# Kernel tuning notes

Hardware: AMD Instinct MI355X
Metric: run time of the kernel (lower is better)

Reference implementation:

```python
import jax, jax.numpy as jnp
import numpy as np

B, L, D = 4, 2048, 1024
H, DK, DV = 16, 64, 64
SCALE = float((4 * DK) ** 0.5)
EPS = 1e-6


def setup_inputs() -> dict:
    key = jax.random.key(0)
    ks = jax.random.split(key, 16)
    s_in = 1.0 / np.sqrt(D)
    inp = {}
    for i, name in enumerate(["q_a", "k_a", "v_a", "q_s", "k_s", "v_s"]):
        inp[name] = jax.random.normal(ks[i], (B, L, D), dtype=jnp.float32)
    # weights stored as [in, out] so projection is x @ W (equivalent math to nn.Linear)
    for j, name in enumerate(["Wqa", "Wka", "Wva", "Wqs", "Wks", "Wvs", "Wfc"]):
        inp[name] = jax.random.normal(ks[6 + j], (D, D), dtype=jnp.float32) * s_in
    inp["gamma"] = jnp.ones((D,), dtype=jnp.float32)
    inp["beta"] = jnp.zeros((D,), dtype=jnp.float32)
    return inp


def _proj(x, W, dh):
    # [B,L,D] @ [D, H*dh] -> [B,H,L,dh]
    return (x @ W).reshape(B, -1, H, dh).transpose(0, 2, 1, 3)


def reference(q_a, k_a, v_a, q_s, k_s, v_s, Wqa, Wka, Wva, Wqs, Wks, Wvs, Wfc, gamma, beta):
    residual = q_a + q_s
    qa = _proj(q_a, Wqa, DK)
    ka = _proj(k_a, Wka, DK)
    va = _proj(v_a, Wva, DV)
    qs = _proj(q_s, Wqs, DK)
    ks_ = _proj(k_s, Wks, DK)
    vs = _proj(v_s, Wvs, DV)
    # a2a + a2s + s2a + s2s == (qa+qs) @ (ka+ks)^T  (algebraic identity)
    q = qa + qs
    k = ka + ks_
    v = va + vs
    scores = jnp.einsum("bhqd,bhkd->bhqk", q, k) / SCALE
    attn = jax.nn.softmax(scores, axis=-1)  # dropout = identity (eval)
    out = jnp.einsum("bhqk,bhkd->bhqd", attn, v)  # [B,H,L,DV]
    out = out.transpose(0, 2, 1, 3).reshape(B, L, H * DV)
    out = out @ Wfc + residual
    mu = jnp.mean(out, axis=-1, keepdims=True)
    var = jnp.var(out, axis=-1, keepdims=True)
    out = (out - mu) * jax.lax.rsqrt(var + EPS) * gamma + beta
    return out
```

## Files before the change

### kernel.cpp

```cpp
#include <hip/hip_runtime.h>
#include <hip/hip_bf16.h>
#include <stdint.h>

typedef __attribute__((ext_vector_type(4))) float f32x4;
typedef __attribute__((ext_vector_type(16))) float f32x16;
typedef __attribute__((ext_vector_type(8))) short short8;
typedef __attribute__((ext_vector_type(2))) int int2v;

#define DEV static __device__ __forceinline__

DEV unsigned short f2bf(float f) {
  unsigned u = __float_as_uint(f);
  u += 0x7fffu + ((u >> 16) & 1u);
  return (unsigned short)(u >> 16);
}

DEV uint32_t cvtpk(float a, float b) {
  uint32_t r;
  asm("v_cvt_pk_bf16_f32 %0, %1, %2" : "=v"(r) : "v"(a), "v"(b));
  return r;
}

DEV int2v pl32(int a, int b) {
  return __builtin_amdgcn_permlane32_swap(a, b, false, false);
}

typedef const __attribute__((address_space(1))) void* gas_ptr;
typedef __attribute__((address_space(3))) void* las_ptr;

DEV void gload_lds16(const void* g, void* l) {
  __builtin_amdgcn_global_load_lds((gas_ptr)g, (las_ptr)l, 16, 0, 0);
}

struct CvtArgs {
  const float* in[6];
  unsigned short* out[6];
};

__global__ __launch_bounds__(256) void cvt_kernel(CvtArgs a, int n4) {
  const float* __restrict__ in = a.in[blockIdx.y];
  unsigned short* __restrict__ out = a.out[blockIdx.y];
  int idx = blockIdx.x * blockDim.x + threadIdx.x;
  int stride = gridDim.x * blockDim.x;
  for (int i = idx; i < n4; i += stride) {
    float4 v = reinterpret_cast<const float4*>(in)[i];
    ushort4 o;
    o.x = f2bf(v.x); o.y = f2bf(v.y); o.z = f2bf(v.z); o.w = f2bf(v.w);
    reinterpret_cast<ushort4*>(out)[i] = o;
  }
}

struct TcvtArgs {
  const float* src[7];
  unsigned short* dst[7];
  int stride[7];
  int koff[7];
};

__global__ __launch_bounds__(256) void tcvt_kernel(TcvtArgs a) {
  const int which = blockIdx.z;
  const float* __restrict__ src = a.src[which];
  unsigned short* __restrict__ dst = a.dst[which];
  const int dstStride = a.stride[which], kOff = a.koff[which];
  __shared__ float tile[32][33];
  int tx = threadIdx.x & 31;
  int ty = threadIdx.x >> 5;
  int n0 = blockIdx.x * 32;
  int k0 = blockIdx.y * 32;
#pragma unroll
  for (int i = 0; i < 4; i++)
    tile[ty + 8 * i][tx] = src[(size_t)(k0 + ty + 8 * i) * 1024 + n0 + tx];
  __syncthreads();
#pragma unroll
  for (int i = 0; i < 4; i++) {
    int n = n0 + ty + 8 * i;
    dst[(size_t)n * dstStride + kOff + k0 + tx] = f2bf(tile[tx][ty + 8 * i]);
  }
}

struct G3Args {
  const unsigned short* A1[3];
  const unsigned short* A2[3];
  const unsigned short* WT[3];
  unsigned short* out[3];
};

__global__ __launch_bounds__(256) void gemm3_kernel(G3Args g) {
  __shared__ unsigned short As[128 * 32];
  __shared__ unsigned short Bs[128 * 32];
  const int orig = blockIdx.x;
  const int swz = (orig & 7) * 192 + (orig >> 3);
  const int which = swz >> 9;
  const int bid = swz & 511;
  const unsigned short* __restrict__ A1 = g.A1[which];
  const unsigned short* __restrict__ A2 = g.A2[which];
  const unsigned short* __restrict__ WT = g.WT[which];
  unsigned short* __restrict__ outp = g.out[which];

  const int tid = threadIdx.x;
  const int lane = tid & 63;
  const int w = tid >> 6;
  const int mt = bid >> 3, nt = bid & 7;
  const int m0 = mt * 128, n0 = nt * 128;

  const int srow = (w << 4) + (lane >> 2);
  const int scol = (lane & 3) << 3;

  f32x4 zero4 = {0.f, 0.f, 0.f, 0.f};
  f32x4 acc[4][4];
#pragma unroll
  for (int mi = 0; mi < 4; mi++)
#pragma unroll
    for (int ni = 0; ni < 4; ni++) acc[mi][ni] = zero4;

  const int wr = w >> 1, wc = w & 1;
  const int arow = (wr << 6) + (lane & 15);
  const int brow = (wc << 6) + (lane & 15);
  const int kcol = (lane >> 4) << 3;

  for (int kt = 0; kt < 64; kt++) {
    const int kk = kt << 5;
    const unsigned short* Asrc;
    int ka;
    if (kk < 1024) { Asrc = A1; ka = kk; } else { Asrc = A2; ka = kk - 1024; }
#pragma unroll
    for (int p = 0; p < 2; p++) {
      const unsigned short* gp = Asrc + (size_t)(m0 + p * 64 + srow) * 1024 + ka + scol;
      gload_lds16(gp, &As[(p * 64 + srow) * 32 + scol]);
    }
#pragma unroll
    for (int p = 0; p < 2; p++) {
      const unsigned short* gp = WT + (size_t)(n0 + p * 64 + srow) * 2048 + kk + scol;
      gload_lds16(gp, &Bs[(p * 64 + srow) * 32 + scol]);
    }
    __syncthreads();

    short8 av[4], bv[4];
#pragma unroll
    for (int mi = 0; mi < 4; mi++)
      av[mi] = *reinterpret_cast<const short8*>(&As[(arow + mi * 16) * 32 + kcol]);
#pragma unroll
    for (int ni = 0; ni < 4; ni++)
      bv[ni] = *reinterpret_cast<const short8*>(&Bs[(brow + ni * 16) * 32 + kcol]);
#pragma unroll
    for (int mi = 0; mi < 4; mi++)
#pragma unroll
      for (int ni = 0; ni < 4; ni++)
        acc[mi][ni] = __builtin_amdgcn_mfma_f32_16x16x32_bf16(av[mi], bv[ni], acc[mi][ni], 0, 0, 0);
    __syncthreads();
  }

#pragma unroll
  for (int mi = 0; mi < 4; mi++) {
#pragma unroll
    for (int ni = 0; ni < 4; ni++) {
      const int col = n0 + (wc << 6) + ni * 16 + (lane & 15);
      const int rbase = m0 + (wr << 6) + mi * 16 + ((lane >> 4) << 2);
      const int h = col >> 6, d = col & 63;
      if (which < 2) {
#pragma unroll
        for (int r = 0; r < 4; r++) {
          const int m = rbase + r;
          const int b = m >> 11, l = m & 2047;
          outp[((size_t)((b * 16 + h) * 2048 + l)) * 64 + d] = f2bf(acc[mi][ni][r]);
        }
      } else {
        const int m = rbase;
        const int b = m >> 11, l = m & 2047;
        const int bh = b * 16 + h;
        ushort4 o;
        o.x = f2bf(acc[mi][ni][0]);
        o.y = f2bf(acc[mi][ni][1]);
        o.z = f2bf(acc[mi][ni][2]);
        o.w = f2bf(acc[mi][ni][3]);
        *reinterpret_cast<ushort4*>(
            outp + (size_t)(bh * 64 + (l >> 5)) * 2048 + d * 32 + (l & 31)) = o;
      }
    }
  }
}

__global__ __launch_bounds__(256) void gemmfc_kernel(const unsigned short* __restrict__ A1,
                                                     const unsigned short* __restrict__ WT,
                                                     const float* __restrict__ qa,
                                                     const float* __restrict__ qs,
                                                     float* __restrict__ outp) {
  __shared__ unsigned short As[128 * 32];
  __shared__ unsigned short Bs[128 * 32];
  const int orig = blockIdx.x;
  const int bid = (orig & 7) * 64 + (orig >> 3);
  const int tid = threadIdx.x;
  const int lane = tid & 63;
  const int w = tid >> 6;
  const int mt = bid >> 3, nt = bid & 7;
  const int m0 = mt * 128, n0 = nt * 128;

  const int srow = (w << 4) + (lane >> 2);
  const int scol = (lane & 3) << 3;

  f32x4 zero4 = {0.f, 0.f, 0.f, 0.f};
  f32x4 acc[4][4];
#pragma unroll
  for (int mi = 0; mi < 4; mi++)
#pragma unroll
    for (int ni = 0; ni < 4; ni++) acc[mi][ni] = zero4;

  const int wr = w >> 1, wc = w & 1;
  const int arow = (wr << 6) + (lane & 15);
  const int brow = (wc << 6) + (lane & 15);
  const int kcol = (lane >> 4) << 3;

  for (int kt = 0; kt < 32; kt++) {
    const int kk = kt << 5;
#pragma unroll
    for (int p = 0; p < 2; p++) {
      const unsigned short* gp = A1 + (size_t)(m0 + p * 64 + srow) * 1024 + kk + scol;
      gload_lds16(gp, &As[(p * 64 + srow) * 32 + scol]);
    }
#pragma unroll
    for (int p = 0; p < 2; p++) {
      const unsigned short* gp = WT + (size_t)(n0 + p * 64 + srow) * 1024 + kk + scol;
      gload_lds16(gp, &Bs[(p * 64 + srow) * 32 + scol]);
    }
    __syncthreads();

    short8 av[4], bv[4];
#pragma unroll
    for (int mi = 0; mi < 4; mi++)
      av[mi] = *reinterpret_cast<const short8*>(&As[(arow + mi * 16) * 32 + kcol]);
#pragma unroll
    for (int ni = 0; ni < 4; ni++)
      bv[ni] = *reinterpret_cast<const short8*>(&Bs[(brow + ni * 16) * 32 + kcol]);
#pragma unroll
    for (int mi = 0; mi < 4; mi++)
#pragma unroll
      for (int ni = 0; ni < 4; ni++)
        acc[mi][ni] = __builtin_amdgcn_mfma_f32_16x16x32_bf16(av[mi], bv[ni], acc[mi][ni], 0, 0, 0);
    __syncthreads();
  }

#pragma unroll
  for (int mi = 0; mi < 4; mi++) {
#pragma unroll
    for (int ni = 0; ni < 4; ni++) {
      const int col = n0 + (wc << 6) + ni * 16 + (lane & 15);
      const int rbase = m0 + (wr << 6) + mi * 16 + ((lane >> 4) << 2);
#pragma unroll
      for (int r = 0; r < 4; r++) {
        const size_t idx = (size_t)(rbase + r) * 1024 + col;
        outp[idx] = acc[mi][ni][r] + qa[idx] + qs[idx];
      }
    }
  }
}

__global__ __launch_bounds__(256) void attn_kernel(const unsigned short* __restrict__ Q,
                                                   const unsigned short* __restrict__ K,
                                                   const unsigned short* __restrict__ Vt,
                                                   unsigned short* __restrict__ O) {
  __shared__ unsigned short Ks[2][2048];
  __shared__ unsigned short Vs[2][2048];
  const int tid = threadIdx.x;
  const int lane = tid & 63;
  const int w = tid >> 6;
  const int n = blockIdx.x;
  const int bh = (n & 7) * 8 + (n >> 7);
  const int qg = (n >> 3) & 15;
  const int q0 = qg * 128 + w * 32;
  const int lo = lane & 31, hi = lane >> 5;

  const unsigned short* qp = Q + ((size_t)bh * 2048 + q0 + lo) * 64 + (hi << 3);
  short8 qf[4];
#pragma unroll
  for (int c = 0; c < 4; c++)
    qf[c] = *reinterpret_cast<const short8*>(qp + c * 16);

  f32x16 o0 = {0.f,0.f,0.f,0.f,0.f,0.f,0.f,0.f,0.f,0.f,0.f,0.f,0.f,0.f,0.f,0.f};
  f32x16 o1 = {0.f,0.f,0.f,0.f,0.f,0.f,0.f,0.f,0.f,0.f,0.f,0.f,0.f,0.f,0.f,0.f};
  float mrun = -1e30f, lsum = 0.0f;
  const float KS = 1.44269504088896f / 16.0f;

  const char* Kg = (const char*)(K + (size_t)bh * 2048 * 64);
  const char* Vg = (const char*)(Vt + (size_t)bh * 131072);

  const int p16 = tid * 16;
  const int lswz = p16 ^ (((p16 >> 7) & 7) << 4);
  const int koff = lswz;
  const int voff = (lswz >> 7) * 64 + ((lswz >> 6) & 1) * 2048 + (lswz & 63);

  const int sK = (lo & 7) << 4;
  int kix[4];
#pragma unroll
  for (int c = 0; c < 4; c++)
    kix[c] = ((lo * 128 + hi * 16 + c * 32) ^ sK) >> 1;
  int vix[4];
  vix[0] = ((lo * 128 + hi * 16) ^ sK) >> 1;
  vix[1] = ((lo * 128 + 32 + hi * 16) ^ sK) >> 1;
  vix[2] = ((lo * 128 + 64 + hi * 16) ^ sK) >> 1;
  vix[3] = ((lo * 128 + 96 + hi * 16) ^ sK) >> 1;

  auto STAGE = [&](int kt, int buf) {
    gload_lds16(Kg + (size_t)kt * 4096 + koff, &Ks[buf][tid * 8]);
    gload_lds16(Vg + (size_t)kt * 4096 + voff, &Vs[buf][tid * 8]);
  };

  STAGE(0, 0);
  __syncthreads();

  for (int kt = 0; kt < 64; kt++) {
    const int buf = kt & 1;
    const int nx = (kt < 63) ? kt + 1 : 63;
    STAGE(nx, buf ^ 1);

    short8 kc[4], vc[4];
#pragma unroll
    for (int c = 0; c < 4; c++)
      kc[c] = *reinterpret_cast<const short8*>(&Ks[buf][kix[c]]);
#pragma unroll
    for (int c = 0; c < 4; c++)
      vc[c] = *reinterpret_cast<const short8*>(&Vs[buf][vix[c]]);

    f32x16 s = {0.f,0.f,0.f,0.f,0.f,0.f,0.f,0.f,0.f,0.f,0.f,0.f,0.f,0.f,0.f,0.f};
    __builtin_amdgcn_s_setprio(1);
#pragma unroll
    for (int c = 0; c < 4; c++)
      s = __builtin_amdgcn_mfma_f32_32x32x16_bf16(kc[c], qf[c], s, 0, 0, 0);
    __builtin_amdgcn_s_setprio(0);

    float m01 = fmaxf(s[0], s[1]), m23 = fmaxf(s[2], s[3]);
    float m45 = fmaxf(s[4], s[5]), m67 = fmaxf(s[6], s[7]);
    float m89 = fmaxf(s[8], s[9]), mab = fmaxf(s[10], s[11]);
    float mcd = fmaxf(s[12], s[13]), mef = fmaxf(s[14], s[15]);
    float cmax = fmaxf(fmaxf(fmaxf(m01, m23), fmaxf(m45, m67)),
                       fmaxf(fmaxf(m89, mab), fmaxf(mcd, mef)));
    {
      int2v mm = pl32(__float_as_int(cmax), __float_as_int(cmax));
      cmax = fmaxf(__int_as_float(mm.x), __int_as_float(mm.y));
    }

    if (__any(cmax > mrun + 128.0f)) {
      const float mnew = fmaxf(mrun, cmax);
      const float alpha = __builtin_amdgcn_exp2f((mrun - mnew) * KS);
      lsum *= alpha;
#pragma unroll
      for (int r = 0; r < 16; r++) {
        const int row = (r & 3) + ((r >> 2) << 3) + (hi << 2);
        const float ar = __shfl(alpha, row);
        o0[r] *= ar;
        o1[r] *= ar;
      }
      mrun = mnew;
    }

    float pr[16];
    const float mk = mrun * KS;
#pragma unroll
    for (int r = 0; r < 16; r++)
      pr[r] = __builtin_amdgcn_exp2f(__builtin_fmaf(s[r], KS, -mk));
    float c01 = (pr[0] + pr[1]) + (pr[2] + pr[3]);
    float c23 = (pr[4] + pr[5]) + (pr[6] + pr[7]);
    float c45 = (pr[8] + pr[9]) + (pr[10] + pr[11]);
    float c67 = (pr[12] + pr[13]) + (pr[14] + pr[15]);
    float csum = (c01 + c23) + (c45 + c67);
    {
      int2v ss = pl32(__float_as_int(csum), __float_as_int(csum));
      csum = __int_as_float(ss.x) + __int_as_float(ss.y);
    }
    lsum += csum;

    const uint32_t c0 = cvtpk(pr[0], pr[1]),   c1 = cvtpk(pr[2], pr[3]);
    const uint32_t c2 = cvtpk(pr[4], pr[5]),   c3 = cvtpk(pr[6], pr[7]);
    const uint32_t c4 = cvtpk(pr[8], pr[9]),   c5 = cvtpk(pr[10], pr[11]);
    const uint32_t c6 = cvtpk(pr[12], pr[13]), c7 = cvtpk(pr[14], pr[15]);
    int2v s02 = pl32((int)c0, (int)c2);
    int2v s13 = pl32((int)c1, (int)c3);
    int2v s46 = pl32((int)c4, (int)c6);
    int2v s57 = pl32((int)c5, (int)c7);
    union { uint32_t u[4]; short8 v; } pa, pb;
    pa.u[0] = (uint32_t)s02.x; pa.u[1] = (uint32_t)s13.x;
    pa.u[2] = (uint32_t)s02.y; pa.u[3] = (uint32_t)s13.y;
    pb.u[0] = (uint32_t)s46.x; pb.u[1] = (uint32_t)s57.x;
    pb.u[2] = (uint32_t)s46.y; pb.u[3] = (uint32_t)s57.y;

    __builtin_amdgcn_s_setprio(1);
    o0 = __builtin_amdgcn_mfma_f32_32x32x16_bf16(pa.v, vc[0], o0, 0, 0, 0);
    o0 = __builtin_amdgcn_mfma_f32_32x32x16_bf16(pb.v, vc[1], o0, 0, 0, 0);
    o1 = __builtin_amdgcn_mfma_f32_32x32x16_bf16(pa.v, vc[2], o1, 0, 0, 0);
    o1 = __builtin_amdgcn_mfma_f32_32x32x16_bf16(pb.v, vc[3], o1, 0, 0, 0);
    __builtin_amdgcn_s_setprio(0);

    __syncthreads();
  }

  const int b = bh >> 4, h = bh & 15;
#pragma unroll
  for (int r = 0; r < 16; r++) {
    const int row = (r & 3) + ((r >> 2) << 3) + (hi << 2);
    const float lr = __shfl(lsum, row);
    const float inv = __builtin_amdgcn_rcpf(lr);
    const size_t base = ((size_t)b * 2048 + q0 + row) * 1024 + h * 64 + lo;
    O[base] = f2bf(o0[r] * inv);
    O[base + 32] = f2bf(o1[r] * inv);
  }
}

__global__ __launch_bounds__(256) void ln_kernel(const float* __restrict__ fc,
                                                 const float* __restrict__ gamma,
                                                 const float* __restrict__ beta,
                                                 float* __restrict__ out) {
  const int m = blockIdx.x;
  const int t = threadIdx.x;
  const size_t base = (size_t)m * 1024 + t * 4;
  float4 x = *reinterpret_cast<const float4*>(fc + base);
  float s1 = x.x + x.y + x.z + x.w;
  float s2 = x.x * x.x + x.y * x.y + x.z * x.z + x.w * x.w;
#pragma unroll
  for (int off = 1; off < 64; off <<= 1) {
    s1 += __shfl_xor(s1, off);
    s2 += __shfl_xor(s2, off);
  }
  __shared__ float sh[8];
  const int w = t >> 6, lane = t & 63;
  if (lane == 0) { sh[w] = s1; sh[4 + w] = s2; }
  __syncthreads();
  s1 = sh[0] + sh[1] + sh[2] + sh[3];
  s2 = sh[4] + sh[5] + sh[6] + sh[7];
  const float mu = s1 * (1.0f / 1024.0f);
  const float var = s2 * (1.0f / 1024.0f) - mu * mu;
  const float rs = rsqrtf(var + 1e-6f);
  const float4 g = *reinterpret_cast<const float4*>(gamma + t * 4);
  const float4 be = *reinterpret_cast<const float4*>(beta + t * 4);
  float4 y;
  y.x = (x.x - mu) * rs * g.x + be.x;
  y.y = (x.y - mu) * rs * g.y + be.y;
  y.z = (x.z - mu) * rs * g.z + be.z;
  y.w = (x.w - mu) * rs * g.w + be.w;
  *reinterpret_cast<float4*>(out + base) = y;
}

__global__ void sentinel_kernel(float* out, int n) {
  int i = blockIdx.x * blockDim.x + threadIdx.x;
  if (i < n) out[i] = 1234.5f;
}

extern "C" void kernel_launch(void* const* d_in, const int* in_sizes, int n_in,
                              void* d_out, int out_size, void* d_ws, size_t ws_size,
                              hipStream_t stream) {
  const size_t MB = 1024ull * 1024ull;
  if (ws_size < 174 * MB) {
    sentinel_kernel<<<(out_size + 255) / 256, 256, 0, stream>>>((float*)d_out, out_size);
    return;
  }
  const float* fin[6];
  for (int i = 0; i < 6; i++) fin[i] = (const float*)d_in[i];
  const float* Wf[7];
  for (int i = 0; i < 7; i++) Wf[i] = (const float*)d_in[6 + i];
  const float* gamma = (const float*)d_in[13];
  const float* beta = (const float*)d_in[14];

  char* ws = (char*)d_ws;
  unsigned short* Abf[6];
  for (int i = 0; i < 6; i++) Abf[i] = (unsigned short*)(ws + (size_t)i * 16 * MB);
  unsigned short* WqT = (unsigned short*)(ws + 96 * MB);
  unsigned short* WkT = (unsigned short*)(ws + 100 * MB);
  unsigned short* WvT = (unsigned short*)(ws + 104 * MB);
  unsigned short* WfcT = (unsigned short*)(ws + 108 * MB);
  unsigned short* Qb = (unsigned short*)(ws + 110 * MB);
  unsigned short* Kb = (unsigned short*)(ws + 126 * MB);
  unsigned short* Vtb = (unsigned short*)(ws + 142 * MB);
  unsigned short* Ob = (unsigned short*)(ws + 158 * MB);
  float* fcout = (float*)(ws + 16 * MB);

  CvtArgs ca;
  for (int i = 0; i < 6; i++) { ca.in[i] = fin[i]; ca.out[i] = Abf[i]; }
  cvt_kernel<<<dim3(1024, 6), 256, 0, stream>>>(ca, 2097152);

  TcvtArgs ta;
  const int wsel[7] = {0, 3, 1, 4, 2, 5, 6};
  unsigned short* wdst[7] = {WqT, WqT, WkT, WkT, WvT, WvT, WfcT};
  for (int i = 0; i < 7; i++) {
    ta.src[i] = Wf[wsel[i]];
    ta.dst[i] = wdst[i];
    ta.stride[i] = (i < 6) ? 2048 : 1024;
    ta.koff[i] = (i < 6) ? ((i & 1) ? 1024 : 0) : 0;
  }
  tcvt_kernel<<<dim3(32, 32, 7), 256, 0, stream>>>(ta);

  G3Args g3;
  g3.A1[0] = Abf[0]; g3.A2[0] = Abf[3]; g3.WT[0] = WqT; g3.out[0] = Qb;
  g3.A1[1] = Abf[1]; g3.A2[1] = Abf[4]; g3.WT[1] = WkT; g3.out[1] = Kb;
  g3.A1[2] = Abf[2]; g3.A2[2] = Abf[5]; g3.WT[2] = WvT; g3.out[2] = Vtb;
  gemm3_kernel<<<1536, 256, 0, stream>>>(g3);

  attn_kernel<<<1024, 256, 0, stream>>>(Qb, Kb, Vtb, Ob);

  gemmfc_kernel<<<512, 256, 0, stream>>>(Ob, WfcT, fin[0], fin[3], fcout);

  ln_kernel<<<8192, 256, 0, stream>>>(fcout, gamma, beta, (float*)d_out);
}
```

Before: 349.4 us.

## Fuse fp32-to-bf16 input conversion into projection GEMM with double-buffered LDS

Removes the separate activation conversion kernel and has the QKV projection GEMM read fp32 inputs directly, converting them to bf16 in registers before writing to LDS. The LDS tiles are double-buffered so the next k-tile's global loads are issued before the current tile's MFMAs. This avoids writing and re-reading a bf16 copy of six activation tensors. In exchange the GEMM reads twice as many bytes per A element, with extra VGPR pressure and conversion ALU work. Each A tile is also reloaded by all 8 N-tile blocks.

```diff
diff --git a/kernel.cpp b/kernel.cpp
--- a/kernel.cpp
+++ b/kernel.cpp
@@ -30,24 +30,6 @@
 
 DEV void gload_lds16(const void* g, void* l) {
   __builtin_amdgcn_global_load_lds((gas_ptr)g, (las_ptr)l, 16, 0, 0);
-}
-
-struct CvtArgs {
-  const float* in[6];
-  unsigned short* out[6];
-};
-
-__global__ __launch_bounds__(256) void cvt_kernel(CvtArgs a, int n4) {
-  const float* __restrict__ in = a.in[blockIdx.y];
-  unsigned short* __restrict__ out = a.out[blockIdx.y];
-  int idx = blockIdx.x * blockDim.x + threadIdx.x;
-  int stride = gridDim.x * blockDim.x;
-  for (int i = idx; i < n4; i += stride) {
-    float4 v = reinterpret_cast<const float4*>(in)[i];
-    ushort4 o;
-    o.x = f2bf(v.x); o.y = f2bf(v.y); o.z = f2bf(v.z); o.w = f2bf(v.w);
-    reinterpret_cast<ushort4*>(out)[i] = o;
-  }
 }
 
 struct TcvtArgs {
@@ -79,21 +61,21 @@
 }
 
 struct G3Args {
-  const unsigned short* A1[3];
-  const unsigned short* A2[3];
+  const float* A1[3];
+  const float* A2[3];
   const unsigned short* WT[3];
   unsigned short* out[3];
 };
 
 __global__ __launch_bounds__(256) void gemm3_kernel(G3Args g) {
-  __shared__ unsigned short As[128 * 32];
-  __shared__ unsigned short Bs[128 * 32];
+  __shared__ unsigned short As[2][128 * 32];
+  __shared__ unsigned short Bs[2][128 * 32];
   const int orig = blockIdx.x;
   const int swz = (orig & 7) * 192 + (orig >> 3);
   const int which = swz >> 9;
   const int bid = swz & 511;
-  const unsigned short* __restrict__ A1 = g.A1[which];
-  const unsigned short* __restrict__ A2 = g.A2[which];
+  const float* __restrict__ A1 = g.A1[which];
+  const float* __restrict__ A2 = g.A2[which];
   const unsigned short* __restrict__ WT = g.WT[which];
   unsigned short* __restrict__ outp = g.out[which];
 
@@ -118,35 +100,68 @@
   const int brow = (wc << 6) + (lane & 15);
   const int kcol = (lane >> 4) << 3;
 
-  for (int kt = 0; kt < 64; kt++) {
+  auto ALOAD = [&](int kt, float4* r) {
     const int kk = kt << 5;
-    const unsigned short* Asrc;
-    int ka;
-    if (kk < 1024) { Asrc = A1; ka = kk; } else { Asrc = A2; ka = kk - 1024; }
+    const float* Af = (kk < 1024) ? A1 : A2;
+    const int ka = kk & 1023;
 #pragma unroll
     for (int p = 0; p < 2; p++) {
-      const unsigned short* gp = Asrc + (size_t)(m0 + p * 64 + srow) * 1024 + ka + scol;
-      gload_lds16(gp, &As[(p * 64 + srow) * 32 + scol]);
-    }
+      const float* gp = Af + (size_t)(m0 + p * 64 + srow) * 1024 + ka + scol;
+      r[2 * p] = *reinterpret_cast<const float4*>(gp);
+      r[2 * p + 1] = *reinterpret_cast<const float4*>(gp + 4);
+    }
+  };
+  auto AWRITE = [&](int buf, const float4* r) {
+#pragma unroll
+    for (int p = 0; p < 2; p++) {
+      union { uint32_t u[4]; short8 v; } pk;
+      pk.u[0] = cvtpk(r[2 * p].x, r[2 * p].y);
+      pk.u[1] = cvtpk(r[2 * p].z, r[2 * p].w);
+      pk.u[2] = cvtpk(r[2 * p + 1].x, r[2 * p + 1].y);
+      pk.u[3] = cvtpk(r[2 * p + 1].z, r[2 * p + 1].w);
+      *reinterpret_cast<short8*>(&As[buf][(p * 64 + srow) * 32 + scol]) = pk.v;
+    }
+  };
+  auto BSTAGE = [&](int kt, int buf) {
+    const int kk = kt << 5;
 #pragma unroll
     for (int p = 0; p < 2; p++) {
       const unsigned short* gp = WT + (size_t)(n0 + p * 64 + srow) * 2048 + kk + scol;
-      gload_lds16(gp, &Bs[(p * 64 + srow) * 32 + scol]);
-    }
+      gload_lds16(gp, &Bs[buf][(p * 64 + srow) * 32 + scol]);
+    }
+  };
+
+  {
+    float4 ar[4];
+    ALOAD(0, ar);
+    BSTAGE(0, 0);
+    AWRITE(0, ar);
     __syncthreads();
+  }
+
+  for (int kt = 0; kt < 64; kt++) {
+    const int cur = kt & 1, nxt = cur ^ 1;
+    float4 an[4];
+    if (kt < 63) {
+      ALOAD(kt + 1, an);
+      BSTAGE(kt + 1, nxt);
+    }
 
     short8 av[4], bv[4];
 #pragma unroll
     for (int mi = 0; mi < 4; mi++)
-      av[mi] = *reinterpret_cast<const short8*>(&As[(arow + mi * 16) * 32 + kcol]);
+      av[mi] = *reinterpret_cast<const short8*>(&As[cur][(arow + mi * 16) * 32 + kcol]);
 #pragma unroll
     for (int ni = 0; ni < 4; ni++)
-      bv[ni] = *reinterpret_cast<const short8*>(&Bs[(brow + ni * 16) * 32 + kcol]);
+      bv[ni] = *reinterpret_cast<const short8*>(&Bs[cur][(brow + ni * 16) * 32 + kcol]);
 #pragma unroll
     for (int mi = 0; mi < 4; mi++)
 #pragma unroll
       for (int ni = 0; ni < 4; ni++)
         acc[mi][ni] = __builtin_amdgcn_mfma_f32_16x16x32_bf16(av[mi], bv[ni], acc[mi][ni], 0, 0, 0);
+
+    __builtin_amdgcn_sched_barrier(0);
+    if (kt < 63) AWRITE(nxt, an);
     __syncthreads();
   }
 
@@ -459,8 +474,6 @@
   const float* beta = (const float*)d_in[14];
 
   char* ws = (char*)d_ws;
-  unsigned short* Abf[6];
-  for (int i = 0; i < 6; i++) Abf[i] = (unsigned short*)(ws + (size_t)i * 16 * MB);
   unsigned short* WqT = (unsigned short*)(ws + 96 * MB);
   unsigned short* WkT = (unsigned short*)(ws + 100 * MB);
   unsigned short* WvT = (unsigned short*)(ws + 104 * MB);
@@ -471,10 +484,6 @@
   unsigned short* Ob = (unsigned short*)(ws + 158 * MB);
   float* fcout = (float*)(ws + 16 * MB);
 
-  CvtArgs ca;
-  for (int i = 0; i < 6; i++) { ca.in[i] = fin[i]; ca.out[i] = Abf[i]; }
-  cvt_kernel<<<dim3(1024, 6), 256, 0, stream>>>(ca, 2097152);
-
   TcvtArgs ta;
   const int wsel[7] = {0, 3, 1, 4, 2, 5, 6};
   unsigned short* wdst[7] = {WqT, WqT, WkT, WkT, WvT, WvT, WfcT};
@@ -487,9 +496,9 @@
   tcvt_kernel<<<dim3(32, 32, 7), 256, 0, stream>>>(ta);
 
   G3Args g3;
-  g3.A1[0] = Abf[0]; g3.A2[0] = Abf[3]; g3.WT[0] = WqT; g3.out[0] = Qb;
-  g3.A1[1] = Abf[1]; g3.A2[1] = Abf[4]; g3.WT[1] = WkT; g3.out[1] = Kb;
-  g3.A1[2] = Abf[2]; g3.A2[2] = Abf[5]; g3.WT[2] = WvT; g3.out[2] = Vtb;
+  g3.A1[0] = fin[0]; g3.A2[0] = fin[3]; g3.WT[0] = WqT; g3.out[0] = Qb;
+  g3.A1[1] = fin[1]; g3.A2[1] = fin[4]; g3.WT[1] = WkT; g3.out[1] = Kb;
+  g3.A1[2] = fin[2]; g3.A2[2] = fin[5]; g3.WT[2] = WvT; g3.out[2] = Vtb;
   gemm3_kernel<<<1536, 256, 0, stream>>>(g3);
 
   attn_kernel<<<1024, 256, 0, stream>>>(Qb, Kb, Vtb, Ob);
```

After: 368.4 us. 1.05x slower.

## Fuse fp32-to-bf16 activation conversion into projection GEMM loads

Applied to the files above, without the earlier changes.

Removes the separate conversion kernel that turned the six fp32 activation tensors into bf16 copies. The projection GEMM now loads fp32 tiles straight into LDS with global_load_lds and converts them to bf16 with v_cvt_pk_bf16_f32 just before the MFMA. This avoids writing and re-reading about 96MB of bf16 intermediates and saves one launch. In exchange, the GEMM reads twice as many A bytes per tile (each tile is reused across the 8 N-tiles), uses double the LDS for A, and does extra conversion work in the inner loop.

```diff
diff --git a/kernel.cpp b/kernel.cpp
--- a/kernel.cpp
+++ b/kernel.cpp
@@ -30,24 +30,6 @@
 
 DEV void gload_lds16(const void* g, void* l) {
   __builtin_amdgcn_global_load_lds((gas_ptr)g, (las_ptr)l, 16, 0, 0);
-}
-
-struct CvtArgs {
-  const float* in[6];
-  unsigned short* out[6];
-};
-
-__global__ __launch_bounds__(256) void cvt_kernel(CvtArgs a, int n4) {
-  const float* __restrict__ in = a.in[blockIdx.y];
-  unsigned short* __restrict__ out = a.out[blockIdx.y];
-  int idx = blockIdx.x * blockDim.x + threadIdx.x;
-  int stride = gridDim.x * blockDim.x;
-  for (int i = idx; i < n4; i += stride) {
-    float4 v = reinterpret_cast<const float4*>(in)[i];
-    ushort4 o;
-    o.x = f2bf(v.x); o.y = f2bf(v.y); o.z = f2bf(v.z); o.w = f2bf(v.w);
-    reinterpret_cast<ushort4*>(out)[i] = o;
-  }
 }
 
 struct TcvtArgs {
@@ -79,21 +61,21 @@
 }
 
 struct G3Args {
-  const unsigned short* A1[3];
-  const unsigned short* A2[3];
+  const float* A1[3];
+  const float* A2[3];
   const unsigned short* WT[3];
   unsigned short* out[3];
 };
 
 __global__ __launch_bounds__(256) void gemm3_kernel(G3Args g) {
-  __shared__ unsigned short As[128 * 32];
+  __shared__ float Asf[128 * 32];
   __shared__ unsigned short Bs[128 * 32];
   const int orig = blockIdx.x;
   const int swz = (orig & 7) * 192 + (orig >> 3);
   const int which = swz >> 9;
   const int bid = swz & 511;
-  const unsigned short* __restrict__ A1 = g.A1[which];
-  const unsigned short* __restrict__ A2 = g.A2[which];
+  const float* __restrict__ A1 = g.A1[which];
+  const float* __restrict__ A2 = g.A2[which];
   const unsigned short* __restrict__ WT = g.WT[which];
   unsigned short* __restrict__ outp = g.out[which];
 
@@ -105,6 +87,8 @@
 
   const int srow = (w << 4) + (lane >> 2);
   const int scol = (lane & 3) << 3;
+  const int farow = tid >> 3;
+  const int facol = (tid & 7) << 2;
 
   f32x4 zero4 = {0.f, 0.f, 0.f, 0.f};
   f32x4 acc[4][4];
@@ -120,14 +104,13 @@
 
   for (int kt = 0; kt < 64; kt++) {
     const int kk = kt << 5;
-    const unsigned short* Asrc;
+    const float* Af;
     int ka;
-    if (kk < 1024) { Asrc = A1; ka = kk; } else { Asrc = A2; ka = kk - 1024; }
-#pragma unroll
-    for (int p = 0; p < 2; p++) {
-      const unsigned short* gp = Asrc + (size_t)(m0 + p * 64 + srow) * 1024 + ka + scol;
-      gload_lds16(gp, &As[(p * 64 + srow) * 32 + scol]);
-    }
+    if (kk < 1024) { Af = A1; ka = kk; } else { Af = A2; ka = kk - 1024; }
+#pragma unroll
+    for (int r = 0; r < 4; r++)
+      gload_lds16(Af + (size_t)(m0 + r * 32 + farow) * 1024 + ka + facol,
+                  &Asf[r * 1024 + tid * 4]);
 #pragma unroll
     for (int p = 0; p < 2; p++) {
       const unsigned short* gp = WT + (size_t)(n0 + p * 64 + srow) * 2048 + kk + scol;
@@ -137,8 +120,16 @@
 
     short8 av[4], bv[4];
 #pragma unroll
-    for (int mi = 0; mi < 4; mi++)
-      av[mi] = *reinterpret_cast<const short8*>(&As[(arow + mi * 16) * 32 + kcol]);
+    for (int mi = 0; mi < 4; mi++) {
+      const float4 lo = *reinterpret_cast<const float4*>(&Asf[(arow + mi * 16) * 32 + kcol]);
+      const float4 hi = *reinterpret_cast<const float4*>(&Asf[(arow + mi * 16) * 32 + kcol + 4]);
+      union { uint32_t u[4]; short8 v; } pk;
+      pk.u[0] = cvtpk(lo.x, lo.y);
+      pk.u[1] = cvtpk(lo.z, lo.w);
+      pk.u[2] = cvtpk(hi.x, hi.y);
+      pk.u[3] = cvtpk(hi.z, hi.w);
+      av[mi] = pk.v;
+    }
 #pragma unroll
     for (int ni = 0; ni < 4; ni++)
       bv[ni] = *reinterpret_cast<const short8*>(&Bs[(brow + ni * 16) * 32 + kcol]);
@@ -459,8 +450,6 @@
   const float* beta = (const float*)d_in[14];
 
   char* ws = (char*)d_ws;
-  unsigned short* Abf[6];
-  for (int i = 0; i < 6; i++) Abf[i] = (unsigned short*)(ws + (size_t)i * 16 * MB);
   unsigned short* WqT = (unsigned short*)(ws + 96 * MB);
   unsigned short* WkT = (unsigned short*)(ws + 100 * MB);
   unsigned short* WvT = (unsigned short*)(ws + 104 * MB);
@@ -471,10 +460,6 @@
   unsigned short* Ob = (unsigned short*)(ws + 158 * MB);
   float* fcout = (float*)(ws + 16 * MB);
 
-  CvtArgs ca;
-  for (int i = 0; i < 6; i++) { ca.in[i] = fin[i]; ca.out[i] = Abf[i]; }
-  cvt_kernel<<<dim3(1024, 6), 256, 0, stream>>>(ca, 2097152);
-
   TcvtArgs ta;
   const int wsel[7] = {0, 3, 1, 4, 2, 5, 6};
   unsigned short* wdst[7] = {WqT, WqT, WkT, WkT, WvT, WvT, WfcT};
@@ -487,9 +472,9 @@
   tcvt_kernel<<<dim3(32, 32, 7), 256, 0, stream>>>(ta);
 
   G3Args g3;
-  g3.A1[0] = Abf[0]; g3.A2[0] = Abf[3]; g3.WT[0] = WqT; g3.out[0] = Qb;
-  g3.A1[1] = Abf[1]; g3.A2[1] = Abf[4]; g3.WT[1] = WkT; g3.out[1] = Kb;
-  g3.A1[2] = Abf[2]; g3.A2[2] = Abf[5]; g3.WT[2] = WvT; g3.out[2] = Vtb;
+  g3.A1[0] = fin[0]; g3.A2[0] = fin[3]; g3.WT[0] = WqT; g3.out[0] = Qb;
+  g3.A1[1] = fin[1]; g3.A2[1] = fin[4]; g3.WT[1] = WkT; g3.out[1] = Kb;
+  g3.A1[2] = fin[2]; g3.A2[2] = fin[5]; g3.WT[2] = WvT; g3.out[2] = Vtb;
   gemm3_kernel<<<1536, 256, 0, stream>>>(g3);
 
   attn_kernel<<<1024, 256, 0, stream>>>(Qb, Kb, Vtb, Ob);
```

New measurement: 373.3 us. +6.9%, slower.
